# Kernel tuning notes

Hardware: AMD Instinct MI355X
Metric: run time of the kernel (lower is better)

The kernel has to match this reference:

```python
import jax, jax.numpy as jnp
import numpy as np

N_NODES = 100000


def _sage_conv(x, src, dst, w_self, w_neigh, b):
    # DGL SAGEConv('mean'): fc_self(x) + fc_neigh(mean of in-neighbor feats) + bias
    msgs = x[src]                                        # [E, d] gather
    agg = jax.ops.segment_sum(msgs, dst, num_segments=N_NODES)   # [N, d]
    deg = jax.ops.segment_sum(jnp.ones_like(dst, dtype=x.dtype), dst,
                              num_segments=N_NODES)      # [N]
    mean = agg / jnp.maximum(deg, 1.0)[:, None]          # zero-degree -> 0
    return x @ w_self + mean @ w_neigh + b


def setup_inputs() -> dict:
    key = jax.random.key(0)
    ks = jax.random.split(key, 8)
    E, D_IN, D_HID, D_OUT = 1000000, 64, 64, 32
    features = jax.random.normal(ks[0], (N_NODES, D_IN), dtype=jnp.float32)
    src = jax.random.randint(ks[1], (E,), 0, N_NODES, dtype=jnp.int32)
    dst = jax.random.randint(ks[2], (E,), 0, N_NODES, dtype=jnp.int32)
    s = lambda k, i, o: jax.random.normal(k, (i, o), dtype=jnp.float32) / np.sqrt(i)
    return {
        "features": features, "src": src, "dst": dst,
        "w_self1": s(ks[3], D_IN, D_HID), "w_neigh1": s(ks[4], D_IN, D_HID),
        "b1": jnp.zeros((D_HID,), jnp.float32),
        "w_self2": s(ks[5], D_HID, D_OUT), "w_neigh2": s(ks[6], D_HID, D_OUT),
        "b2": jnp.zeros((D_OUT,), jnp.float32),
    }


def reference(features, src, dst, w_self1, w_neigh1, b1, w_self2, w_neigh2, b2):
    h = _sage_conv(features, src, dst, w_self1, w_neigh1, b1)
    h = jax.nn.relu(h)
    # dropout: identity (inference mode)
    h = _sage_conv(h, src, dst, w_self2, w_neigh2, b2)
    return h
```

## Files before the change

### kernel.cpp

```cpp
#include <hip/hip_runtime.h>


#define SPAN        128
#define SPAN_SHIFT  7
#define PART_BLOCK  1024
#define PART_EPT    4
#define NBMAX       1024
#define LDS_S       72

typedef __attribute__((ext_vector_type(8))) short bf16x8;
typedef __attribute__((ext_vector_type(4))) float f32x4;

__device__ __forceinline__ unsigned bf16_rne(float f) {
    unsigned u = __float_as_uint(f);
    return (u + 0x7FFFu + ((u >> 16) & 1u)) >> 16;
}
__device__ __forceinline__ float bf_lo(unsigned u) { return __uint_as_float(u << 16); }
__device__ __forceinline__ float bf_hi(unsigned u) { return __uint_as_float(u & 0xFFFF0000u); }

__global__ __launch_bounds__(PART_BLOCK) void k_partition(
    const int* __restrict__ src, const int* __restrict__ dst,
    int* __restrict__ cursor, unsigned int* __restrict__ pairs,
    int E, int cap,
    const float* __restrict__ feat, unsigned short* __restrict__ xh, long total8,
    const float* __restrict__ ws1, const float* __restrict__ wn1,
    const float* __restrict__ ws2, const float* __restrict__ wn2,
    unsigned short* __restrict__ wt)
{
    const int tid = threadIdx.x;
    for (long i = (long)blockIdx.x * PART_BLOCK + tid; i < total8;
         i += (long)gridDim.x * PART_BLOCK) {
        const float4 a = ((const float4*)feat)[i * 2];
        const float4 b = ((const float4*)feat)[i * 2 + 1];
        uint4 o;
        o.x = bf16_rne(a.x) | (bf16_rne(a.y) << 16);
        o.y = bf16_rne(a.z) | (bf16_rne(a.w) << 16);
        o.z = bf16_rne(b.x) | (bf16_rne(b.y) << 16);
        o.w = bf16_rne(b.z) | (bf16_rne(b.w) << 16);
        ((uint4*)xh)[i] = o;
    }
    if (blockIdx.x < 12) {
        int j = blockIdx.x * PART_BLOCK + tid;
        int mat = j >> 12, rem = j & 4095;
        int c = rem >> 6, k = rem & 63;
        float v;
        if (mat == 0)      v = ws1[k * 64 + c];
        else if (mat == 1) v = wn1[k * 64 + c];
        else               v = (c < 32) ? wn2[k * 32 + c] : ws2[k * 32 + (c - 32)];
        wt[(mat << 12) + (c << 6) + k] = (unsigned short)bf16_rne(v);
    }

    __shared__ int cnt[NBMAX];
    __shared__ int gbase[NBMAX];
    __shared__ int lcur[NBMAX];
    cnt[tid] = 0; lcur[tid] = 0;
    __syncthreads();

    int sv[PART_EPT], bv[PART_EPT];
    const int e0 = blockIdx.x * (PART_BLOCK * PART_EPT) + tid;
    #pragma unroll
    for (int j = 0; j < PART_EPT; ++j) {
        int e = e0 + j * PART_BLOCK;
        bv[j] = -1;
        if (e < E) {
            int s = src[e], d = dst[e];
            bv[j] = d >> SPAN_SHIFT;
            sv[j] = s | ((d & (SPAN - 1)) << 24);
            atomicAdd(&cnt[bv[j]], 1);
        }
    }
    __syncthreads();
    if (cnt[tid] > 0) gbase[tid] = atomicAdd(&cursor[tid], cnt[tid]);
    __syncthreads();
    #pragma unroll
    for (int j = 0; j < PART_EPT; ++j) {
        if (bv[j] >= 0) {
            int r = gbase[bv[j]] + atomicAdd(&lcur[bv[j]], 1);
            if (r < cap) pairs[(size_t)bv[j] * cap + r] = (unsigned int)sv[j];
        }
    }
}

__global__ __launch_bounds__(256) void k_bucket_csr(
    unsigned int* __restrict__ pairs,
    const int* __restrict__ cursor,
    int* __restrict__ starts, int* __restrict__ degs,
    int N, int cap)
{
    __shared__ int cnt[SPAN];
    __shared__ int pref[SPAN];
    __shared__ int lcur[SPAN];
    extern __shared__ unsigned int sorted[];
    const int tid = threadIdx.x;
    const int b = blockIdx.x;
    if (tid < SPAN) { cnt[tid] = 0; lcur[tid] = 0; }
    __syncthreads();

    int m = cursor[b]; if (m > cap) m = cap;
    const size_t pb = (size_t)b * cap;

    for (int i = tid; i < m; i += 256)
        atomicAdd(&cnt[pairs[pb + i] >> 24], 1);
    __syncthreads();

    if (tid < SPAN) pref[tid] = cnt[tid];
    __syncthreads();
    for (int off = 1; off < SPAN; off <<= 1) {
        int v = 0;
        if (tid < SPAN && tid >= off) v = pref[tid - off];
        __syncthreads();
        if (tid < SPAN) pref[tid] += v;
        __syncthreads();
    }

    for (int i = tid; i < m; i += 256) {
        unsigned int p = pairs[pb + i];
        int r = p >> 24;
        int base = (r == 0) ? 0 : pref[r - 1];
        int pos = base + atomicAdd(&lcur[r], 1);
        sorted[pos] = p & 0xFFFFFFu;
    }
    __syncthreads();
    for (int i = tid; i < m; i += 256) pairs[pb + i] = sorted[i];
    if (tid < SPAN) {
        int node = (b << SPAN_SHIFT) + tid;
        if (node < N) {
            int base = (tid == 0) ? 0 : pref[tid - 1];
            starts[node] = (int)pb + base;
            degs[node]   = cnt[tid];
        }
    }
}

__global__ __launch_bounds__(256) void k_fused(
    const unsigned short* __restrict__ xh,
    const unsigned int* __restrict__ esrc,
    const int* __restrict__ starts, const int* __restrict__ degs,
    const unsigned short* __restrict__ wt,
    const float* __restrict__ b1, const float* __restrict__ b2,
    unsigned short* __restrict__ t2,
    float* __restrict__ outp,
    int n)
{
    __shared__ __align__(16) unsigned short sX[128 * LDS_S];
    __shared__ __align__(16) unsigned short sWt[3 * 64 * LDS_S];
    const int tid  = threadIdx.x;
    const int w    = tid >> 6, lane = tid & 63;
    const int quad = lane >> 4, lm = lane & 15;
    const int gm0  = blockIdx.x * 128;
    const int rowA = w * 32;

    for (int i = tid; i < 1536; i += 256) {
        int r  = i >> 3;
        int k0 = (i & 7) << 3;
        *(uint4*)&sWt[r * LDS_S + k0] = *(const uint4*)&wt[(r << 6) + k0];
    }
    for (int i = lane; i < 256; i += 64) {
        int m = rowA + (i >> 3), k0 = (i & 7) << 3;
        int gm = gm0 + m;
        uint4 v = make_uint4(0, 0, 0, 0);
        if (gm < n) v = *(const uint4*)&xh[(size_t)gm * 64 + k0];
        *(uint4*)&sX[m * LDS_S + k0] = v;
    }
    __syncthreads();

    f32x4 acc[2][4];
    #pragma unroll
    for (int mt = 0; mt < 2; ++mt)
        #pragma unroll
        for (int nt = 0; nt < 4; ++nt) acc[mt][nt] = (f32x4){0.f, 0.f, 0.f, 0.f};

    #pragma unroll
    for (int kt = 0; kt < 2; ++kt) {
        bf16x8 a0 = *(const bf16x8*)&sX[(rowA + lm) * LDS_S + kt * 32 + quad * 8];
        bf16x8 a1 = *(const bf16x8*)&sX[(rowA + 16 + lm) * LDS_S + kt * 32 + quad * 8];
        #pragma unroll
        for (int nt = 0; nt < 4; ++nt) {
            bf16x8 b = *(const bf16x8*)&sWt[(nt * 16 + lm) * LDS_S + kt * 32 + quad * 8];
            acc[0][nt] = __builtin_amdgcn_mfma_f32_16x16x32_bf16(a0, b, acc[0][nt], 0, 0, 0);
            acc[1][nt] = __builtin_amdgcn_mfma_f32_16x16x32_bf16(a1, b, acc[1][nt], 0, 0, 0);
        }
    }

    for (int grp = 0; grp < 8; ++grp) {
        const int v0 = gm0 + rowA + grp * 4;
        int e[4], end[4], dg[4];
        #pragma unroll
        for (int j = 0; j < 4; ++j) {
            int v = v0 + j;
            if (v < n) { int b = starts[v]; dg[j] = degs[v]; e[j] = b + quad; end[j] = b + dg[j]; }
            else { dg[j] = 0; e[j] = 0; end[j] = 0; }
        }
        float ga[4][4];
        #pragma unroll
        for (int j = 0; j < 4; ++j)
            #pragma unroll
            for (int k = 0; k < 4; ++k) ga[j][k] = 0.f;

        while ((e[0] < end[0]) | (e[1] < end[1]) | (e[2] < end[2]) | (e[3] < end[3])) {
            uint2 u[4]; float m[4];
            #pragma unroll
            for (int j = 0; j < 4; ++j) {
                bool p = e[j] < end[j];
                m[j] = p ? 1.f : 0.f;
                int idx = p ? e[j] : 0;
                int s = (int)(esrc[idx] & 0xFFFFFFu);
                s = s < n ? s : n - 1;
                u[j] = *(const uint2*)&xh[(size_t)s * 64 + lm * 4];
            }
            #pragma unroll
            for (int j = 0; j < 4; ++j) {
                ga[j][0] = fmaf(m[j], bf_lo(u[j].x), ga[j][0]);
                ga[j][1] = fmaf(m[j], bf_hi(u[j].x), ga[j][1]);
                ga[j][2] = fmaf(m[j], bf_lo(u[j].y), ga[j][2]);
                ga[j][3] = fmaf(m[j], bf_hi(u[j].y), ga[j][3]);
                e[j] += 4;
            }
        }
        #pragma unroll
        for (int j = 0; j < 4; ++j) {
            #pragma unroll
            for (int d = 16; d <= 32; d <<= 1) {
                #pragma unroll
                for (int k = 0; k < 4; ++k) ga[j][k] += __shfl_xor(ga[j][k], d);
            }
            if (lane < 16 && v0 + j < n) {
                float f = dg[j] ? 1.f / (float)dg[j] : 0.f;
                uint2 o;
                o.x = bf16_rne(ga[j][0] * f) | (bf16_rne(ga[j][1] * f) << 16);
                o.y = bf16_rne(ga[j][2] * f) | (bf16_rne(ga[j][3] * f) << 16);
                *(uint2*)&sX[(rowA + grp * 4 + j) * LDS_S + lm * 4] = o;
            }
        }
    }

    #pragma unroll
    for (int kt = 0; kt < 2; ++kt) {
        bf16x8 a0 = *(const bf16x8*)&sX[(rowA + lm) * LDS_S + kt * 32 + quad * 8];
        bf16x8 a1 = *(const bf16x8*)&sX[(rowA + 16 + lm) * LDS_S + kt * 32 + quad * 8];
        #pragma unroll
        for (int nt = 0; nt < 4; ++nt) {
            bf16x8 b = *(const bf16x8*)&sWt[(64 + nt * 16 + lm) * LDS_S + kt * 32 + quad * 8];
            acc[0][nt] = __builtin_amdgcn_mfma_f32_16x16x32_bf16(a0, b, acc[0][nt], 0, 0, 0);
            acc[1][nt] = __builtin_amdgcn_mfma_f32_16x16x32_bf16(a1, b, acc[1][nt], 0, 0, 0);
        }
    }

    #pragma unroll
    for (int nt = 0; nt < 4; ++nt) {
        float bb = b1[nt * 16 + lm];
        #pragma unroll
        for (int mt = 0; mt < 2; ++mt) {
            int rbase = rowA + mt * 16 + quad * 4;
            #pragma unroll
            for (int r = 0; r < 4; ++r) {
                float hv = fmaxf(acc[mt][nt][r] + bb, 0.f);
                sX[(rbase + r) * LDS_S + nt * 16 + lm] = (unsigned short)bf16_rne(hv);
            }
        }
    }

    f32x4 acc2[2][4];
    #pragma unroll
    for (int mt = 0; mt < 2; ++mt)
        #pragma unroll
        for (int nt = 0; nt < 4; ++nt) acc2[mt][nt] = (f32x4){0.f, 0.f, 0.f, 0.f};
    #pragma unroll
    for (int kt = 0; kt < 2; ++kt) {
        bf16x8 a0 = *(const bf16x8*)&sX[(rowA + lm) * LDS_S + kt * 32 + quad * 8];
        bf16x8 a1 = *(const bf16x8*)&sX[(rowA + 16 + lm) * LDS_S + kt * 32 + quad * 8];
        #pragma unroll
        for (int nt = 0; nt < 4; ++nt) {
            bf16x8 b = *(const bf16x8*)&sWt[(128 + nt * 16 + lm) * LDS_S + kt * 32 + quad * 8];
            acc2[0][nt] = __builtin_amdgcn_mfma_f32_16x16x32_bf16(a0, b, acc2[0][nt], 0, 0, 0);
            acc2[1][nt] = __builtin_amdgcn_mfma_f32_16x16x32_bf16(a1, b, acc2[1][nt], 0, 0, 0);
        }
    }

    #pragma unroll
    for (int mt = 0; mt < 2; ++mt) {
        int rbase = gm0 + rowA + mt * 16 + quad * 4;
        #pragma unroll
        for (int nt = 0; nt < 2; ++nt) {
            #pragma unroll
            for (int r = 0; r < 4; ++r) {
                int gm = rbase + r;
                if (gm < n)
                    t2[(size_t)gm * 32 + nt * 16 + lm] =
                        (unsigned short)bf16_rne(acc2[mt][nt][r]);
            }
        }
        #pragma unroll
        for (int nt = 2; nt < 4; ++nt) {
            float bb = b2[(nt - 2) * 16 + lm];
            #pragma unroll
            for (int r = 0; r < 4; ++r) {
                int gm = rbase + r;
                if (gm < n)
                    outp[(size_t)gm * 32 + (nt - 2) * 16 + lm] = acc2[mt][nt][r] + bb;
            }
        }
    }
}

__global__ __launch_bounds__(256) void k_gather_b32add(
    const unsigned short* __restrict__ t2,
    const unsigned int* __restrict__ esrc,
    const int* __restrict__ starts, const int* __restrict__ degs,
    float* __restrict__ outp, int n)
{
    const int w = threadIdx.x >> 6, lane = threadIdx.x & 63;
    const int g = lane >> 3, c = lane & 7;
    const int v0 = (blockIdx.x * 4 + w) * 4;
    if (v0 >= n) return;

    int e[4], end[4], deg[4];
    #pragma unroll
    for (int j = 0; j < 4; ++j) {
        int v = v0 + j;
        if (v < n) { int b = starts[v]; deg[j] = degs[v]; e[j] = b + g; end[j] = b + deg[j]; }
        else { deg[j] = 0; e[j] = 0; end[j] = 0; }
    }
    float acc[4][4];
    #pragma unroll
    for (int j = 0; j < 4; ++j)
        #pragma unroll
        for (int k = 0; k < 4; ++k) acc[j][k] = 0.f;

    while ((e[0] < end[0]) | (e[1] < end[1]) | (e[2] < end[2]) | (e[3] < end[3])) {
        uint2 u[4]; float m[4];
        #pragma unroll
        for (int j = 0; j < 4; ++j) {
            bool p = e[j] < end[j];
            m[j] = p ? 1.f : 0.f;
            int idx = p ? e[j] : 0;
            int s = (int)(esrc[idx] & 0xFFFFFFu);
            s = s < n ? s : n - 1;
            u[j] = *(const uint2*)&t2[(size_t)s * 32 + c * 4];
        }
        #pragma unroll
        for (int j = 0; j < 4; ++j) {
            acc[j][0] = fmaf(m[j], bf_lo(u[j].x), acc[j][0]);
            acc[j][1] = fmaf(m[j], bf_hi(u[j].x), acc[j][1]);
            acc[j][2] = fmaf(m[j], bf_lo(u[j].y), acc[j][2]);
            acc[j][3] = fmaf(m[j], bf_hi(u[j].y), acc[j][3]);
            e[j] += 8;
        }
    }
    #pragma unroll
    for (int j = 0; j < 4; ++j) {
        #pragma unroll
        for (int d = 8; d <= 32; d <<= 1) {
            #pragma unroll
            for (int k = 0; k < 4; ++k) acc[j][k] += __shfl_xor(acc[j][k], d);
        }
        if (lane < 8 && v0 + j < n && deg[j] > 0) {
            float f = 1.f / (float)deg[j];
            float4 o = *(const float4*)&outp[(size_t)(v0 + j) * 32 + c * 4];
            o.x += acc[j][0] * f; o.y += acc[j][1] * f;
            o.z += acc[j][2] * f; o.w += acc[j][3] * f;
            *(float4*)&outp[(size_t)(v0 + j) * 32 + c * 4] = o;
        }
    }
}

extern "C" void kernel_launch(void* const* d_in, const int* in_sizes, int n_in,
                              void* d_out, int out_size, void* d_ws, size_t ws_size,
                              hipStream_t stream) {
    const float* feat = (const float*)d_in[0];
    const int*   src  = (const int*)d_in[1];
    const int*   dst  = (const int*)d_in[2];
    const float* ws1  = (const float*)d_in[3];
    const float* wn1  = (const float*)d_in[4];
    const float* b1   = (const float*)d_in[5];
    const float* ws2  = (const float*)d_in[6];
    const float* wn2  = (const float*)d_in[7];
    const float* b2   = (const float*)d_in[8];
    float* out = (float*)d_out;

    const int N = in_sizes[0] / 64;
    const int E = in_sizes[1];
    const int nB = (N + SPAN - 1) >> SPAN_SHIFT;

    int cap = ((E + nB - 1) / nB);
    cap = ((cap + cap / 4) + 63) & ~63;
    {
        size_t fixedBytes = NBMAX * 4 + 3 * 4096 * 2 + (size_t)N * 8
                          + (size_t)N * 64 * 2
                          + (size_t)N * 32 * 2
                          + 16384;
        size_t remain = (ws_size > fixedBytes) ? (ws_size - fixedBytes) : 0;
        size_t capMax = remain / ((size_t)nB * 4);
        if ((size_t)cap > capMax) cap = (int)(capMax & ~(size_t)3);
    }

    char* base = (char*)d_ws;
    int* cursor = (int*)base;
    unsigned short* wt = (unsigned short*)(base + NBMAX * 4);
    unsigned int* pairs = (unsigned int*)(base + NBMAX * 4 + 24576);
    size_t sOff = ((size_t)NBMAX * 4 + 24576 + (size_t)nB * cap * 4 + 4096 + 255) & ~(size_t)255;
    int* starts = (int*)(base + sOff);
    int* degs   = starts + N;
    size_t mOff = (sOff + (size_t)N * 8 + 255) & ~(size_t)255;
    unsigned short* xh = (unsigned short*)(base + mOff);
    unsigned short* t2 = xh + (size_t)N * 64;

    hipMemsetAsync(cursor, 0, NBMAX * 4, stream);

    const long total8 = (long)N * 64 / 8;
    const int pblocks = (E + PART_BLOCK * PART_EPT - 1) / (PART_BLOCK * PART_EPT);
    k_partition<<<pblocks, PART_BLOCK, 0, stream>>>(
        src, dst, cursor, pairs, E, cap,
        feat, xh, total8, ws1, wn1, ws2, wn2, wt);
    k_bucket_csr<<<nB, 256, (size_t)cap * 4, stream>>>(pairs, cursor, starts, degs, N, cap);

    const int gblocks = (N + 15) / 16;
    const int tblocks = (N + 127) / 128;

    k_fused<<<tblocks, 256, 0, stream>>>(xh, pairs, starts, degs, wt, b1, b2, t2, out, N);
    k_gather_b32add<<<gblocks, 256, 0, stream>>>(t2, pairs, starts, degs, out, N);
}
```

Baseline: 223.0 us.

## Shrink fused SAGE kernel LDS and use 512 threads with per-wave 16-row tiles

The fused layer kernel no longer stages the three weight matrices and the self-feature tile in LDS. It reads MFMA B operands and the self A operand straight from global memory (cache-resident), and keeps only the aggregated-mean tile in LDS. Blocks grow to 512 threads so each wave owns 16 rows instead of 32, which halves per-wave accumulators and gather work. The goal is higher occupancy and more parallel gather latency hiding, at the cost of repeated global and L1 weight loads per wave and no block-level barrier.

```diff
diff --git a/kernel.cpp b/kernel.cpp
--- a/kernel.cpp
+++ b/kernel.cpp
@@ -132,7 +132,7 @@
     }
 }
 
-__global__ __launch_bounds__(256) void k_fused(
+__global__ __launch_bounds__(512, 6) void k_fused(
     const unsigned short* __restrict__ xh,
     const unsigned int* __restrict__ esrc,
     const int* __restrict__ starts, const int* __restrict__ degs,
@@ -142,48 +142,15 @@
     float* __restrict__ outp,
     int n)
 {
-    __shared__ __align__(16) unsigned short sX[128 * LDS_S];
-    __shared__ __align__(16) unsigned short sWt[3 * 64 * LDS_S];
+    __shared__ __align__(16) unsigned short sM[128 * LDS_S];
     const int tid  = threadIdx.x;
     const int w    = tid >> 6, lane = tid & 63;
     const int quad = lane >> 4, lm = lane & 15;
     const int gm0  = blockIdx.x * 128;
-    const int rowA = w * 32;
-
-    for (int i = tid; i < 1536; i += 256) {
-        int r  = i >> 3;
-        int k0 = (i & 7) << 3;
-        *(uint4*)&sWt[r * LDS_S + k0] = *(const uint4*)&wt[(r << 6) + k0];
-    }
-    for (int i = lane; i < 256; i += 64) {
-        int m = rowA + (i >> 3), k0 = (i & 7) << 3;
-        int gm = gm0 + m;
-        uint4 v = make_uint4(0, 0, 0, 0);
-        if (gm < n) v = *(const uint4*)&xh[(size_t)gm * 64 + k0];
-        *(uint4*)&sX[m * LDS_S + k0] = v;
-    }
-    __syncthreads();
-
-    f32x4 acc[2][4];
-    #pragma unroll
-    for (int mt = 0; mt < 2; ++mt)
-        #pragma unroll
-        for (int nt = 0; nt < 4; ++nt) acc[mt][nt] = (f32x4){0.f, 0.f, 0.f, 0.f};
-
-    #pragma unroll
-    for (int kt = 0; kt < 2; ++kt) {
-        bf16x8 a0 = *(const bf16x8*)&sX[(rowA + lm) * LDS_S + kt * 32 + quad * 8];
-        bf16x8 a1 = *(const bf16x8*)&sX[(rowA + 16 + lm) * LDS_S + kt * 32 + quad * 8];
-        #pragma unroll
-        for (int nt = 0; nt < 4; ++nt) {
-            bf16x8 b = *(const bf16x8*)&sWt[(nt * 16 + lm) * LDS_S + kt * 32 + quad * 8];
-            acc[0][nt] = __builtin_amdgcn_mfma_f32_16x16x32_bf16(a0, b, acc[0][nt], 0, 0, 0);
-            acc[1][nt] = __builtin_amdgcn_mfma_f32_16x16x32_bf16(a1, b, acc[1][nt], 0, 0, 0);
-        }
-    }
-
-    for (int grp = 0; grp < 8; ++grp) {
-        const int v0 = gm0 + rowA + grp * 4;
+    const int rowW = w * 16;
+
+    for (int grp = 0; grp < 4; ++grp) {
+        const int v0 = gm0 + rowW + grp * 4;
         int e[4], end[4], dg[4];
         #pragma unroll
         for (int j = 0; j < 4; ++j) {
@@ -229,57 +196,56 @@
                 uint2 o;
                 o.x = bf16_rne(ga[j][0] * f) | (bf16_rne(ga[j][1] * f) << 16);
                 o.y = bf16_rne(ga[j][2] * f) | (bf16_rne(ga[j][3] * f) << 16);
-                *(uint2*)&sX[(rowA + grp * 4 + j) * LDS_S + lm * 4] = o;
-            }
-        }
-    }
-
+                *(uint2*)&sM[(rowW + grp * 4 + j) * LDS_S + lm * 4] = o;
+            }
+        }
+    }
+
+    f32x4 acc[4];
+    #pragma unroll
+    for (int nt = 0; nt < 4; ++nt) acc[nt] = (f32x4){0.f, 0.f, 0.f, 0.f};
+
+    const int rowG = gm0 + rowW + lm;
+    const int rA = rowG < n ? rowG : n - 1;
     #pragma unroll
     for (int kt = 0; kt < 2; ++kt) {
-        bf16x8 a0 = *(const bf16x8*)&sX[(rowA + lm) * LDS_S + kt * 32 + quad * 8];
-        bf16x8 a1 = *(const bf16x8*)&sX[(rowA + 16 + lm) * LDS_S + kt * 32 + quad * 8];
+        bf16x8 a  = *(const bf16x8*)&xh[(size_t)rA * 64 + kt * 32 + quad * 8];
+        bf16x8 am = *(const bf16x8*)&sM[(rowW + lm) * LDS_S + kt * 32 + quad * 8];
         #pragma unroll
         for (int nt = 0; nt < 4; ++nt) {
-            bf16x8 b = *(const bf16x8*)&sWt[(64 + nt * 16 + lm) * LDS_S + kt * 32 + quad * 8];
-            acc[0][nt] = __builtin_amdgcn_mfma_f32_16x16x32_bf16(a0, b, acc[0][nt], 0, 0, 0);
-            acc[1][nt] = __builtin_amdgcn_mfma_f32_16x16x32_bf16(a1, b, acc[1][nt], 0, 0, 0);
+            bf16x8 bs = *(const bf16x8*)&wt[((nt * 16 + lm) << 6) + kt * 32 + quad * 8];
+            bf16x8 bn = *(const bf16x8*)&wt[(1 << 12) + ((nt * 16 + lm) << 6) + kt * 32 + quad * 8];
+            acc[nt] = __builtin_amdgcn_mfma_f32_16x16x32_bf16(a,  bs, acc[nt], 0, 0, 0);
+            acc[nt] = __builtin_amdgcn_mfma_f32_16x16x32_bf16(am, bn, acc[nt], 0, 0, 0);
         }
     }
 
     #pragma unroll
     for (int nt = 0; nt < 4; ++nt) {
         float bb = b1[nt * 16 + lm];
-        #pragma unroll
-        for (int mt = 0; mt < 2; ++mt) {
-            int rbase = rowA + mt * 16 + quad * 4;
-            #pragma unroll
-            for (int r = 0; r < 4; ++r) {
-                float hv = fmaxf(acc[mt][nt][r] + bb, 0.f);
-                sX[(rbase + r) * LDS_S + nt * 16 + lm] = (unsigned short)bf16_rne(hv);
-            }
-        }
-    }
-
-    f32x4 acc2[2][4];
-    #pragma unroll
-    for (int mt = 0; mt < 2; ++mt)
-        #pragma unroll
-        for (int nt = 0; nt < 4; ++nt) acc2[mt][nt] = (f32x4){0.f, 0.f, 0.f, 0.f};
+        int rbase = rowW + quad * 4;
+        #pragma unroll
+        for (int r = 0; r < 4; ++r) {
+            float hv = fmaxf(acc[nt][r] + bb, 0.f);
+            sM[(rbase + r) * LDS_S + nt * 16 + lm] = (unsigned short)bf16_rne(hv);
+        }
+    }
+
+    f32x4 acc2[4];
+    #pragma unroll
+    for (int nt = 0; nt < 4; ++nt) acc2[nt] = (f32x4){0.f, 0.f, 0.f, 0.f};
     #pragma unroll
     for (int kt = 0; kt < 2; ++kt) {
-        bf16x8 a0 = *(const bf16x8*)&sX[(rowA + lm) * LDS_S + kt * 32 + quad * 8];
-        bf16x8 a1 = *(const bf16x8*)&sX[(rowA + 16 + lm) * LDS_S + kt * 32 + quad * 8];
+        bf16x8 a = *(const bf16x8*)&sM[(rowW + lm) * LDS_S + kt * 32 + quad * 8];
         #pragma unroll
         for (int nt = 0; nt < 4; ++nt) {
-            bf16x8 b = *(const bf16x8*)&sWt[(128 + nt * 16 + lm) * LDS_S + kt * 32 + quad * 8];
-            acc2[0][nt] = __builtin_amdgcn_mfma_f32_16x16x32_bf16(a0, b, acc2[0][nt], 0, 0, 0);
-            acc2[1][nt] = __builtin_amdgcn_mfma_f32_16x16x32_bf16(a1, b, acc2[1][nt], 0, 0, 0);
-        }
-    }
-
-    #pragma unroll
-    for (int mt = 0; mt < 2; ++mt) {
-        int rbase = gm0 + rowA + mt * 16 + quad * 4;
+            bf16x8 b = *(const bf16x8*)&wt[(2 << 12) + ((nt * 16 + lm) << 6) + kt * 32 + quad * 8];
+            acc2[nt] = __builtin_amdgcn_mfma_f32_16x16x32_bf16(a, b, acc2[nt], 0, 0, 0);
+        }
+    }
+
+    {
+        int rbase = gm0 + rowW + quad * 4;
         #pragma unroll
         for (int nt = 0; nt < 2; ++nt) {
             #pragma unroll
@@ -287,7 +253,7 @@
                 int gm = rbase + r;
                 if (gm < n)
                     t2[(size_t)gm * 32 + nt * 16 + lm] =
-                        (unsigned short)bf16_rne(acc2[mt][nt][r]);
+                        (unsigned short)bf16_rne(acc2[nt][r]);
             }
         }
         #pragma unroll
@@ -297,7 +263,7 @@
             for (int r = 0; r < 4; ++r) {
                 int gm = rbase + r;
                 if (gm < n)
-                    outp[(size_t)gm * 32 + (nt - 2) * 16 + lm] = acc2[mt][nt][r] + bb;
+                    outp[(size_t)gm * 32 + (nt - 2) * 16 + lm] = acc2[nt][r] + bb;
             }
         }
     }
@@ -417,6 +383,6 @@
     const int gblocks = (N + 15) / 16;
     const int tblocks = (N + 127) / 128;
 
-    k_fused<<<tblocks, 256, 0, stream>>>(xh, pairs, starts, degs, wt, b1, b2, t2, out, N);
+    k_fused<<<tblocks, 512, 0, stream>>>(xh, pairs, starts, degs, wt, b1, b2, t2, out, N);
     k_gather_b32add<<<gblocks, 256, 0, stream>>>(t2, pairs, starts, degs, out, N);
 }
```

Measured after the change: 199.0 us. 1.12x faster.
